# Performance work log

Measured on AMD Instinct MI355X. Metric: run time of the kernel, lower is better.

## Reference

```python
import jax, jax.numpy as jnp
import numpy as np

N = 50000
IN_C = 512
HID = 16
HEADS = 3
OUT_C = 128
NEG_SLOPE = 0.2


def _add_self_loops(edge_index, n):
    loop = jnp.arange(n, dtype=edge_index.dtype)
    src = jnp.concatenate([edge_index[0], loop])
    dst = jnp.concatenate([edge_index[1], loop])
    return src, dst


def gat_conv(x, W, a_src, a_dst, b, src, dst, n):
    # x: [N, Fin], W: [Fin, H*C], a_src/a_dst: [H, C], b: [H*C]
    H, C = a_src.shape
    h = (x @ W).reshape(n, H, C)                      # [N, H, C]
    e_src = jnp.einsum('nhc,hc->nh', h, a_src)        # [N, H]
    e_dst = jnp.einsum('nhc,hc->nh', h, a_dst)        # [N, H]
    e = jax.nn.leaky_relu(e_src[src] + e_dst[dst], NEG_SLOPE)  # [E, H]
    # segment softmax over incoming edges of each destination node
    m = jax.ops.segment_max(e, dst, num_segments=n)
    e = jnp.exp(e - m[dst])
    s = jax.ops.segment_sum(e, dst, num_segments=n)
    alpha = e / s[dst]                                 # [E, H]
    out = jax.ops.segment_sum(h[src] * alpha[:, :, None], dst, num_segments=n)
    return out.reshape(n, H * C) + b


def gcn_conv(x, W, b, src, dst, n):
    h = x @ W                                          # [N, Fout]
    ones = jnp.ones(src.shape[0], dtype=h.dtype)
    deg = jax.ops.segment_sum(ones, dst, num_segments=n)
    dinv = jax.lax.rsqrt(jnp.maximum(deg, 1.0))
    norm = dinv[src] * dinv[dst]                       # [E]
    out = jax.ops.segment_sum(h[src] * norm[:, None], dst, num_segments=n)
    return out + b


def setup_inputs() -> dict:
    key = jax.random.key(0)
    ks = jax.random.split(key, 16)
    E = 800000
    x = jax.random.normal(ks[0], (N, IN_C), dtype=jnp.float32)
    edge_index = jax.random.randint(ks[1], (2, E), 0, N, dtype=jnp.int64)

    def glorot(k, shape):
        fan = shape[0] + shape[-1]
        return jax.random.uniform(k, shape, jnp.float32, -1.0, 1.0) * np.sqrt(6.0 / fan)

    return {
        'x': x,
        'edge_index': edge_index,
        'W1': glorot(ks[2], (IN_C, HEADS * HID)),
        'a_src1': glorot(ks[3], (HEADS, HID)),
        'a_dst1': glorot(ks[4], (HEADS, HID)),
        'b1': jnp.zeros((HEADS * HID,), jnp.float32),
        'W2': glorot(ks[5], (HEADS * HID, OUT_C)),
        'a_src2': glorot(ks[6], (1, OUT_C)),
        'a_dst2': glorot(ks[7], (1, OUT_C)),
        'b2': jnp.zeros((OUT_C,), jnp.float32),
        'Wg': glorot(ks[8], (OUT_C, OUT_C)),
        'bg': jnp.zeros((OUT_C,), jnp.float32),
        'Wl': glorot(ks[9], (OUT_C, OUT_C)),
        'bl': jnp.zeros((OUT_C,), jnp.float32),
    }


def reference(x, edge_index, W1, a_src1, a_dst1, b1, W2, a_src2, a_dst2, b2, Wg, bg, Wl, bl):
    n = x.shape[0]
    src, dst = _add_self_loops(edge_index, n)
    # GATModel: gat1 (3 heads, concat) -> elu -> gat2 (1 head) -> log_softmax
    h = gat_conv(x, W1, a_src1, a_dst1, b1, src, dst, n)
    h = jax.nn.elu(h)
    h = gat_conv(h, W2, a_src2, a_dst2, b2, src, dst, n)
    h = jax.nn.log_softmax(h, axis=1)
    # GCN: only conv1 is used in its forward, followed by relu
    h = jax.nn.relu(gcn_conv(h, Wg, bg, src, dst, n))
    # Linear1
    return h @ Wl + bl
```

## Files before the change

kernel.cpp:

```cpp
#include <hip/hip_runtime.h>
#include <hip/hip_bf16.h>
#include <math.h>

#define NN 50000
#define EE 800000
#define ET 850000
#define NB 196
#define NEG 0.2f

static __device__ __forceinline__ float lrelu(float x){ return x > 0.f ? x : NEG * x; }
static __device__ __forceinline__ void edge_sd(const int* __restrict__ ei, int e, int& s, int& d){
  if (e < EE){ s = ei[e]; d = ei[e + EE]; } else { s = e - EE; d = s; }
}

__global__ __launch_bounds__(256) void k_hist(const int* __restrict__ ei, int* __restrict__ deg_i)
{
  int e = blockIdx.x * 256 + threadIdx.x;
  if (e >= ET) return;
  int s, d; edge_sd(ei, e, s, d);
  atomicAdd(deg_i + d, 1);
}

__global__ __launch_bounds__(256) void k_scan_part(const int* __restrict__ deg_i, int* __restrict__ bsum)
{
  __shared__ int wsum[4];
  int t = threadIdx.x;
  int i = blockIdx.x * 256 + t;
  int v = (i < NN) ? deg_i[i] : 0;
  int r = v;
#pragma unroll
  for (int off = 32; off; off >>= 1) r += __shfl_xor(r, off);
  if ((t & 63) == 0) wsum[t >> 6] = r;
  __syncthreads();
  if (t == 0) bsum[blockIdx.x] = wsum[0] + wsum[1] + wsum[2] + wsum[3];
}

__global__ __launch_bounds__(256) void k_scan_top(const int* __restrict__ bsum, int* __restrict__ boff)
{
  __shared__ int bs[256];
  int t = threadIdx.x;
  int v = (t < NB) ? bsum[t] : 0;
  bs[t] = v;
  __syncthreads();
  for (int off = 1; off < 256; off <<= 1){
    int add = (t >= off) ? bs[t - off] : 0;
    __syncthreads();
    bs[t] += add;
    __syncthreads();
  }
  if (t < NB) boff[t] = bs[t] - v;
}

__global__ __launch_bounds__(256) void k_scan_fin(const int* __restrict__ deg_i,
    const int* __restrict__ boff, int* __restrict__ row_start, float* __restrict__ dinv)
{
  __shared__ int bs[256];
  int t = threadIdx.x;
  int i = blockIdx.x * 256 + t;
  int v = (i < NN) ? deg_i[i] : 0;
  bs[t] = v;
  __syncthreads();
  for (int off = 1; off < 256; off <<= 1){
    int add = (t >= off) ? bs[t - off] : 0;
    __syncthreads();
    bs[t] += add;
    __syncthreads();
  }
  if (i < NN){
    row_start[i] = boff[blockIdx.x] + bs[t] - v;
    dinv[i] = rsqrtf(fmaxf((float)v, 1.0f));
  }
  if (i == 0) row_start[NN] = ET;
}

__global__ __launch_bounds__(256) void k_fill(const int* __restrict__ ei,
    const int* __restrict__ row_start, int* __restrict__ cur, int* __restrict__ csr)
{
  int e = blockIdx.x * 256 + threadIdx.x;
  if (e >= ET) return;
  int s, d; edge_sd(ei, e, s, d);
  int pos = atomicAdd(cur + d, 1);
  csr[row_start[d] + pos] = s;
}

__global__ __launch_bounds__(64) void k_w2(const float* __restrict__ W2,
    const float* __restrict__ as2, const float* __restrict__ ad2,
    float* __restrict__ w2as, float* __restrict__ w2ad)
{
  int k = threadIdx.x;
  if (k >= 48) return;
  float s = 0.f, d = 0.f;
  for (int j = 0; j < 128; ++j){
    float w = W2[(size_t)k * 128 + j];
    s = fmaf(w, as2[j], s);
    d = fmaf(w, ad2[j], d);
  }
  w2as[k] = s; w2ad[k] = d;
}

__global__ __launch_bounds__(256) void k_gat1_gemm(
    const float* __restrict__ x, const float* __restrict__ W1,
    const float* __restrict__ as1, const float* __restrict__ ad1,
    float* __restrict__ h1, float* __restrict__ es1, float* __restrict__ ed1)
{
  __shared__ float Xs[64][68];
  __shared__ float Bs[64][52];
  int t = threadIdx.x;
  int tx = t & 15, ty = t >> 4;
  int n0 = blockIdx.x * 64;
  float acc[4][3] = {};
  for (int kt = 0; kt < 512; kt += 64){
    __syncthreads();
#pragma unroll
    for (int p = 0; p < 4; ++p){
      int f = t + p * 256;
      int node = f >> 4, kq = f & 15;
      float4 v = make_float4(0.f, 0.f, 0.f, 0.f);
      int gn = n0 + node;
      if (gn < NN) v = *(const float4*)(x + (size_t)gn * 512 + kt + kq * 4);
      *(float4*)&Xs[node][kq * 4] = v;
    }
#pragma unroll
    for (int p = 0; p < 3; ++p){
      int f = t + p * 256;
      int k = f / 12, oq = f % 12;
      *(float4*)&Bs[k][oq * 4] = *(const float4*)(W1 + (size_t)(kt + k) * 48 + oq * 4);
    }
    __syncthreads();
#pragma unroll 4
    for (int k4 = 0; k4 < 64; k4 += 4){
      float4 q0 = *(const float4*)&Xs[ty * 4 + 0][k4];
      float4 q1 = *(const float4*)&Xs[ty * 4 + 1][k4];
      float4 q2 = *(const float4*)&Xs[ty * 4 + 2][k4];
      float4 q3 = *(const float4*)&Xs[ty * 4 + 3][k4];
      float a0[4] = {q0.x, q0.y, q0.z, q0.w};
      float a1[4] = {q1.x, q1.y, q1.z, q1.w};
      float a2[4] = {q2.x, q2.y, q2.z, q2.w};
      float a3[4] = {q3.x, q3.y, q3.z, q3.w};
#pragma unroll
      for (int kk = 0; kk < 4; ++kk){
        float b0 = Bs[k4 + kk][tx * 3 + 0];
        float b1 = Bs[k4 + kk][tx * 3 + 1];
        float b2 = Bs[k4 + kk][tx * 3 + 2];
        acc[0][0] = fmaf(a0[kk], b0, acc[0][0]); acc[0][1] = fmaf(a0[kk], b1, acc[0][1]); acc[0][2] = fmaf(a0[kk], b2, acc[0][2]);
        acc[1][0] = fmaf(a1[kk], b0, acc[1][0]); acc[1][1] = fmaf(a1[kk], b1, acc[1][1]); acc[1][2] = fmaf(a1[kk], b2, acc[1][2]);
        acc[2][0] = fmaf(a2[kk], b0, acc[2][0]); acc[2][1] = fmaf(a2[kk], b1, acc[2][1]); acc[2][2] = fmaf(a2[kk], b2, acc[2][2]);
        acc[3][0] = fmaf(a3[kk], b0, acc[3][0]); acc[3][1] = fmaf(a3[kk], b1, acc[3][1]); acc[3][2] = fmaf(a3[kk], b2, acc[3][2]);
      }
    }
  }
#pragma unroll
  for (int i = 0; i < 4; ++i){
    int gn = n0 + ty * 4 + i;
    float ps0 = 0.f, ps1 = 0.f, ps2 = 0.f, pd0 = 0.f, pd1 = 0.f, pd2 = 0.f;
#pragma unroll
    for (int j = 0; j < 3; ++j){
      int o = tx * 3 + j;
      int h = o >> 4;
      float a = acc[i][j];
      float vs = a * as1[o], vd = a * ad1[o];
      if (h == 0){ ps0 += vs; pd0 += vd; }
      else if (h == 1){ ps1 += vs; pd1 += vd; }
      else { ps2 += vs; pd2 += vd; }
    }
#pragma unroll
    for (int off = 1; off < 16; off <<= 1){
      ps0 += __shfl_xor(ps0, off, 16); ps1 += __shfl_xor(ps1, off, 16); ps2 += __shfl_xor(ps2, off, 16);
      pd0 += __shfl_xor(pd0, off, 16); pd1 += __shfl_xor(pd1, off, 16); pd2 += __shfl_xor(pd2, off, 16);
    }
    if (gn < NN){
      float* o = h1 + (size_t)gn * 48 + tx * 3;
      o[0] = acc[i][0]; o[1] = acc[i][1]; o[2] = acc[i][2];
      if (tx == 0){
        es1[(size_t)gn * 3 + 0] = ps0; es1[(size_t)gn * 3 + 1] = ps1; es1[(size_t)gn * 3 + 2] = ps2;
        ed1[(size_t)gn * 3 + 0] = pd0; ed1[(size_t)gn * 3 + 1] = pd1; ed1[(size_t)gn * 3 + 2] = pd2;
      }
    }
  }
}

__global__ __launch_bounds__(256) void k_gat1_agg(
    const int* __restrict__ csr, const int* __restrict__ row_start,
    const float* __restrict__ es1, const float* __restrict__ ed1,
    const float* __restrict__ h1, const float* __restrict__ b1,
    const float* __restrict__ w2as, const float* __restrict__ w2ad,
    float* __restrict__ o1, float* __restrict__ es2, float* __restrict__ ed2)
{
  int dn = (blockIdx.x * 256 + threadIdx.x) >> 6;
  int lane = threadIdx.x & 63;
  if (dn >= NN) return;
  bool act = lane < 48;
  int hd = act ? (lane >> 4) : 0;
  int beg = row_start[dn], end = row_start[dn + 1];
  float edv = ed1[(size_t)dn * 3 + hd];
  float m = -INFINITY, sum = 0.f, acc = 0.f;
  int i = beg;
  for (; i + 1 < end; i += 2){
    int s0 = csr[i], s1 = csr[i + 1];
    float e0 = lrelu(es1[(size_t)s0 * 3 + hd] + edv);
    float e1 = lrelu(es1[(size_t)s1 * 3 + hd] + edv);
    float h0 = act ? h1[(size_t)s0 * 48 + lane] : 0.f;
    float h1v = act ? h1[(size_t)s1 * 48 + lane] : 0.f;
    float mn = fmaxf(m, fmaxf(e0, e1));
    float sc = __expf(m - mn), w0 = __expf(e0 - mn), w1 = __expf(e1 - mn);
    sum = sum * sc + w0 + w1;
    acc = acc * sc + h0 * w0 + h1v * w1;
    m = mn;
  }
  if (i < end){
    int s0 = csr[i];
    float e0 = lrelu(es1[(size_t)s0 * 3 + hd] + edv);
    float h0 = act ? h1[(size_t)s0 * 48 + lane] : 0.f;
    float mn = fmaxf(m, e0);
    float sc = __expf(m - mn), w0 = __expf(e0 - mn);
    sum = sum * sc + w0;
    acc = acc * sc + h0 * w0;
  }
  float v = 0.f;
  if (act){
    v = acc / sum + b1[lane];
    v = v > 0.f ? v : expm1f(v);
    o1[(size_t)dn * 48 + lane] = v;
  }
  float ps = act ? v * w2as[lane] : 0.f;
  float pd = act ? v * w2ad[lane] : 0.f;
#pragma unroll
  for (int off = 32; off; off >>= 1){ ps += __shfl_xor(ps, off); pd += __shfl_xor(pd, off); }
  if (lane == 0){ es2[dn] = ps; ed2[dn] = pd; }
}

__global__ __launch_bounds__(256) void k_gat2_agg(
    const int* __restrict__ csr, const int* __restrict__ row_start,
    const float* __restrict__ es2, const float* __restrict__ ed2,
    const float* __restrict__ o1, float* __restrict__ agg2)
{
  int dn = (blockIdx.x * 256 + threadIdx.x) >> 6;
  int lane = threadIdx.x & 63;
  if (dn >= NN) return;
  bool act = lane < 48;
  int beg = row_start[dn], end = row_start[dn + 1];
  float edv = ed2[dn];
  float m = -INFINITY, sum = 0.f, acc = 0.f;
  int i = beg;
  for (; i + 1 < end; i += 2){
    int s0 = csr[i], s1 = csr[i + 1];
    float e0 = lrelu(es2[s0] + edv);
    float e1 = lrelu(es2[s1] + edv);
    float h0 = act ? o1[(size_t)s0 * 48 + lane] : 0.f;
    float h1v = act ? o1[(size_t)s1 * 48 + lane] : 0.f;
    float mn = fmaxf(m, fmaxf(e0, e1));
    float sc = __expf(m - mn), w0 = __expf(e0 - mn), w1 = __expf(e1 - mn);
    sum = sum * sc + w0 + w1;
    acc = acc * sc + h0 * w0 + h1v * w1;
    m = mn;
  }
  if (i < end){
    int s0 = csr[i];
    float e0 = lrelu(es2[s0] + edv);
    float h0 = act ? o1[(size_t)s0 * 48 + lane] : 0.f;
    float mn = fmaxf(m, e0);
    float sc = __expf(m - mn), w0 = __expf(e0 - mn);
    sum = sum * sc + w0;
    acc = acc * sc + h0 * w0;
  }
  if (act) agg2[(size_t)dn * 48 + lane] = acc / sum;
}

__global__ __launch_bounds__(256) void k_gat2_post(const float* __restrict__ agg2,
    const float* __restrict__ W2, const float* __restrict__ b2, float* __restrict__ o2)
{
  __shared__ float As[64][52];
  __shared__ float Ws[48][128];
  int t = threadIdx.x, tx = t & 15, ty = t >> 4;
  int n0 = blockIdx.x * 64;
#pragma unroll
  for (int p = 0; p < 3; ++p){
    int f = t + p * 256;
    int node = f / 12, kq = f % 12;
    float4 v = make_float4(0.f, 0.f, 0.f, 0.f);
    if (n0 + node < NN) v = *(const float4*)(agg2 + (size_t)(n0 + node) * 48 + kq * 4);
    *(float4*)&As[node][kq * 4] = v;
  }
#pragma unroll
  for (int p = 0; p < 6; ++p){
    int f = t + p * 256;
    int k = f >> 5, cq = f & 31;
    *(float4*)&Ws[k][cq * 4] = *(const float4*)(W2 + (size_t)k * 128 + cq * 4);
  }
  __syncthreads();
  float acc[4][8] = {};
#pragma unroll 4
  for (int k = 0; k < 48; ++k){
    float a0 = As[ty * 4 + 0][k];
    float a1 = As[ty * 4 + 1][k];
    float a2 = As[ty * 4 + 2][k];
    float a3 = As[ty * 4 + 3][k];
    float4 c0 = *(const float4*)&Ws[k][tx * 4];
    float4 c1 = *(const float4*)&Ws[k][tx * 4 + 64];
    float bv[8] = {c0.x, c0.y, c0.z, c0.w, c1.x, c1.y, c1.z, c1.w};
#pragma unroll
    for (int j = 0; j < 8; ++j){
      acc[0][j] = fmaf(a0, bv[j], acc[0][j]);
      acc[1][j] = fmaf(a1, bv[j], acc[1][j]);
      acc[2][j] = fmaf(a2, bv[j], acc[2][j]);
      acc[3][j] = fmaf(a3, bv[j], acc[3][j]);
    }
  }
  float bb[8];
#pragma unroll
  for (int j = 0; j < 4; ++j){ bb[j] = b2[tx * 4 + j]; bb[4 + j] = b2[64 + tx * 4 + j]; }
#pragma unroll
  for (int i = 0; i < 4; ++i){
    int gn = n0 + ty * 4 + i;
    float v[8];
#pragma unroll
    for (int j = 0; j < 8; ++j) v[j] = acc[i][j] + bb[j];
    float mx = v[0];
#pragma unroll
    for (int j = 1; j < 8; ++j) mx = fmaxf(mx, v[j]);
#pragma unroll
    for (int off = 1; off < 16; off <<= 1) mx = fmaxf(mx, __shfl_xor(mx, off, 16));
    float es = 0.f;
#pragma unroll
    for (int j = 0; j < 8; ++j) es += __expf(v[j] - mx);
#pragma unroll
    for (int off = 1; off < 16; off <<= 1) es += __shfl_xor(es, off, 16);
    float lse = mx + __logf(es);
    if (gn < NN){
      float4 o0 = make_float4(v[0] - lse, v[1] - lse, v[2] - lse, v[3] - lse);
      float4 o1v = make_float4(v[4] - lse, v[5] - lse, v[6] - lse, v[7] - lse);
      *(float4*)(o2 + (size_t)gn * 128 + tx * 4) = o0;
      *(float4*)(o2 + (size_t)gn * 128 + tx * 4 + 64) = o1v;
    }
  }
}

__global__ __launch_bounds__(256) void k_gcn_agg(
    const int* __restrict__ csr, const int* __restrict__ row_start,
    const float* __restrict__ dinv, const float* __restrict__ o2,
    float* __restrict__ aggD)
{
  int wid = (blockIdx.x * 256 + threadIdx.x) >> 6;
  int lane = threadIdx.x & 63;
  int half = lane >> 5, l32 = lane & 31;
  int d = wid * 2 + half;
  if (d >= NN) return;
  int beg = row_start[d], end = row_start[d + 1];
  float ax = 0.f, ay = 0.f, az = 0.f, aw = 0.f;
  float bx = 0.f, by = 0.f, bz = 0.f, bw = 0.f;
  int i = beg;
  for (; i + 1 < end; i += 2){
    int s0 = csr[i], s1 = csr[i + 1];
    float d0 = dinv[s0], d1 = dinv[s1];
    float4 v0 = *(const float4*)(o2 + (size_t)s0 * 128 + l32 * 4);
    float4 v1 = *(const float4*)(o2 + (size_t)s1 * 128 + l32 * 4);
    ax = fmaf(v0.x, d0, ax); ay = fmaf(v0.y, d0, ay); az = fmaf(v0.z, d0, az); aw = fmaf(v0.w, d0, aw);
    bx = fmaf(v1.x, d1, bx); by = fmaf(v1.y, d1, by); bz = fmaf(v1.z, d1, bz); bw = fmaf(v1.w, d1, bw);
  }
  if (i < end){
    int s0 = csr[i];
    float d0 = dinv[s0];
    float4 v0 = *(const float4*)(o2 + (size_t)s0 * 128 + l32 * 4);
    ax = fmaf(v0.x, d0, ax); ay = fmaf(v0.y, d0, ay); az = fmaf(v0.z, d0, az); aw = fmaf(v0.w, d0, aw);
  }
  float dd = dinv[d];
  float4 ov = make_float4((ax + bx) * dd, (ay + by) * dd, (az + bz) * dd, (aw + bw) * dd);
  *(float4*)(aggD + (size_t)d * 128 + l32 * 4) = ov;
}

__global__ __launch_bounds__(256) void k_final(const float* __restrict__ aggD,
    const float* __restrict__ Wg, const float* __restrict__ bg,
    const float* __restrict__ Wl, const float* __restrict__ bl,
    float* __restrict__ out)
{
  __shared__ float Ta[64][132];
  __shared__ float Ws[32][128];
  int t = threadIdx.x, tx = t & 15, ty = t >> 4;
  int n0 = blockIdx.x * 64;
#pragma unroll
  for (int p = 0; p < 8; ++p){
    int f = t + p * 256;
    int node = f >> 5, cq = f & 31;
    float4 v = make_float4(0.f, 0.f, 0.f, 0.f);
    if (n0 + node < NN) v = *(const float4*)(aggD + (size_t)(n0 + node) * 128 + cq * 4);
    *(float4*)&Ta[node][cq * 4] = v;
  }
  float accv[4][8];
  const float* Wcur = Wg;
  for (int ph = 0; ph < 2; ++ph){
#pragma unroll
    for (int i = 0; i < 4; ++i)
#pragma unroll
      for (int j = 0; j < 8; ++j) accv[i][j] = 0.f;
    for (int kt = 0; kt < 128; kt += 32){
      __syncthreads();
#pragma unroll
      for (int p = 0; p < 4; ++p){
        int f = t + p * 256;
        int k = f >> 5, cq = f & 31;
        *(float4*)&Ws[k][cq * 4] = *(const float4*)(Wcur + (size_t)(kt + k) * 128 + cq * 4);
      }
      __syncthreads();
#pragma unroll 4
      for (int k = 0; k < 32; ++k){
        float a0 = Ta[ty * 4 + 0][kt + k];
        float a1 = Ta[ty * 4 + 1][kt + k];
        float a2 = Ta[ty * 4 + 2][kt + k];
        float a3 = Ta[ty * 4 + 3][kt + k];
        float4 c0 = *(const float4*)&Ws[k][tx * 4];
        float4 c1 = *(const float4*)&Ws[k][tx * 4 + 64];
        float bv[8] = {c0.x, c0.y, c0.z, c0.w, c1.x, c1.y, c1.z, c1.w};
#pragma unroll
        for (int j = 0; j < 8; ++j){
          accv[0][j] = fmaf(a0, bv[j], accv[0][j]);
          accv[1][j] = fmaf(a1, bv[j], accv[1][j]);
          accv[2][j] = fmaf(a2, bv[j], accv[2][j]);
          accv[3][j] = fmaf(a3, bv[j], accv[3][j]);
        }
      }
    }
    if (ph == 0){
      __syncthreads();
#pragma unroll
      for (int i = 0; i < 4; ++i){
        int nloc = ty * 4 + i;
        float4 w0, w1;
        w0.x = fmaxf(accv[i][0] + bg[tx * 4 + 0], 0.f);
        w0.y = fmaxf(accv[i][1] + bg[tx * 4 + 1], 0.f);
        w0.z = fmaxf(accv[i][2] + bg[tx * 4 + 2], 0.f);
        w0.w = fmaxf(accv[i][3] + bg[tx * 4 + 3], 0.f);
        w1.x = fmaxf(accv[i][4] + bg[64 + tx * 4 + 0], 0.f);
        w1.y = fmaxf(accv[i][5] + bg[64 + tx * 4 + 1], 0.f);
        w1.z = fmaxf(accv[i][6] + bg[64 + tx * 4 + 2], 0.f);
        w1.w = fmaxf(accv[i][7] + bg[64 + tx * 4 + 3], 0.f);
        *(float4*)&Ta[nloc][tx * 4] = w0;
        *(float4*)&Ta[nloc][tx * 4 + 64] = w1;
      }
      Wcur = Wl;
    }
  }
#pragma unroll
  for (int i = 0; i < 4; ++i){
    int gn = n0 + ty * 4 + i;
    if (gn < NN){
      float4 o0, o1v;
      o0.x = accv[i][0] + bl[tx * 4 + 0];
      o0.y = accv[i][1] + bl[tx * 4 + 1];
      o0.z = accv[i][2] + bl[tx * 4 + 2];
      o0.w = accv[i][3] + bl[tx * 4 + 3];
      o1v.x = accv[i][4] + bl[64 + tx * 4 + 0];
      o1v.y = accv[i][5] + bl[64 + tx * 4 + 1];
      o1v.z = accv[i][6] + bl[64 + tx * 4 + 2];
      o1v.w = accv[i][7] + bl[64 + tx * 4 + 3];
      *(float4*)(out + (size_t)gn * 128 + tx * 4) = o0;
      *(float4*)(out + (size_t)gn * 128 + tx * 4 + 64) = o1v;
    }
  }
}

extern "C" void kernel_launch(void* const* d_in, const int* in_sizes, int n_in,
                              void* d_out, int out_size, void* d_ws, size_t ws_size,
                              hipStream_t stream)
{
  const float* x   = (const float*)d_in[0];
  const int*   ei  = (const int*)d_in[1];
  const float* W1  = (const float*)d_in[2];
  const float* as1 = (const float*)d_in[3];
  const float* ad1 = (const float*)d_in[4];
  const float* b1  = (const float*)d_in[5];
  const float* W2  = (const float*)d_in[6];
  const float* as2 = (const float*)d_in[7];
  const float* ad2 = (const float*)d_in[8];
  const float* b2  = (const float*)d_in[9];
  const float* Wg  = (const float*)d_in[10];
  const float* bg  = (const float*)d_in[11];
  const float* Wl  = (const float*)d_in[12];
  const float* bl  = (const float*)d_in[13];
  float* out = (float*)d_out;

  float* ws = (float*)d_ws;
  const size_t n = NN;
  float* h1   = ws;
  float* o1   = ws + 48 * n;
  float* agg2 = ws + 96 * n;
  float* o2   = ws + 144 * n;
  float* aggD = ws + 272 * n;
  float* es1  = ws + 400 * n;
  float* ed1  = ws + 403 * n;
  float* es2  = ws + 406 * n;
  float* ed2  = ws + 407 * n;
  float* dinv = ws + 408 * n;
  float* w2as = ws + 409 * n;
  float* w2ad = ws + 409 * n + 64;
  int* ints   = (int*)(ws + 410 * n);
  int* deg_i     = ints;
  int* cur       = ints + n;
  int* row_start = ints + 2 * n;
  int* csr       = ints + 3 * n + 1;
  int* bsum      = ints + 3 * n + 1 + ET;
  int* boff      = ints + 3 * n + 1 + ET + NB;

  hipMemsetAsync(deg_i, 0, 2 * n * sizeof(int), stream);

  const int egrid = (ET + 255) / 256;
  const int wgrid = (NN * 64) / 256;
  const int hgrid = (NN / 2 * 64) / 256;
  const int ggrid = (NN + 63) / 64;
  k_hist<<<egrid, 256, 0, stream>>>(ei, deg_i);
  k_scan_part<<<NB, 256, 0, stream>>>(deg_i, bsum);
  k_scan_top<<<1, 256, 0, stream>>>(bsum, boff);
  k_scan_fin<<<NB, 256, 0, stream>>>(deg_i, boff, row_start, dinv);
  k_fill<<<egrid, 256, 0, stream>>>(ei, row_start, cur, csr);
  k_w2<<<1, 64, 0, stream>>>(W2, as2, ad2, w2as, w2ad);
  k_gat1_gemm<<<ggrid, 256, 0, stream>>>(x, W1, as1, ad1, h1, es1, ed1);
  k_gat1_agg<<<wgrid, 256, 0, stream>>>(csr, row_start, es1, ed1, h1, b1, w2as, w2ad, o1, es2, ed2);
  k_gat2_agg<<<wgrid, 256, 0, stream>>>(csr, row_start, es2, ed2, o1, agg2);
  k_gat2_post<<<ggrid, 256, 0, stream>>>(agg2, W2, b2, o2);
  k_gcn_agg<<<hgrid, 256, 0, stream>>>(csr, row_start, dinv, o2, aggD);
  k_final<<<ggrid, 256, 0, stream>>>(aggD, Wg, bg, Wl, bl, out);
}
```

Baseline: 563.9 us.

## Prefetch GEMM tiles into registers, fold k_w2 into scan, init cursors from row_start

The GAT1 GEMM and the final two-GEMM kernel now load the next K tile from global memory into registers while the current shared-memory tile is being computed, to hide load latency. The final kernel's two phases are flattened into one 8-chunk loop so the prefetch carries across the switch from Wg to Wl. The W2·a projection moves into the single-block scan_top kernel, which removes one launch. The fill cursors now start at row_start, which drops one indexed load per edge and halves the memset. Register prefetching raises register pressure and may lower occupancy.

Result: slower. 599.1 us (+6.2%).

```diff
diff --git a/kernel.cpp b/kernel.cpp
--- a/kernel.cpp
+++ b/kernel.cpp
@@ -35,7 +35,9 @@
   if (t == 0) bsum[blockIdx.x] = wsum[0] + wsum[1] + wsum[2] + wsum[3];
 }
 
-__global__ __launch_bounds__(256) void k_scan_top(const int* __restrict__ bsum, int* __restrict__ boff)
+__global__ __launch_bounds__(256) void k_scan_top(const int* __restrict__ bsum, int* __restrict__ boff,
+    const float* __restrict__ W2, const float* __restrict__ as2, const float* __restrict__ ad2,
+    float* __restrict__ w2as, float* __restrict__ w2ad)
 {
   __shared__ int bs[256];
   int t = threadIdx.x;
@@ -49,10 +51,20 @@
     __syncthreads();
   }
   if (t < NB) boff[t] = bs[t] - v;
+  if (t < 48){
+    float s = 0.f, d = 0.f;
+    for (int j = 0; j < 128; ++j){
+      float w = W2[(size_t)t * 128 + j];
+      s = fmaf(w, as2[j], s);
+      d = fmaf(w, ad2[j], d);
+    }
+    w2as[t] = s; w2ad[t] = d;
+  }
 }
 
 __global__ __launch_bounds__(256) void k_scan_fin(const int* __restrict__ deg_i,
-    const int* __restrict__ boff, int* __restrict__ row_start, float* __restrict__ dinv)
+    const int* __restrict__ boff, int* __restrict__ row_start, int* __restrict__ cur,
+    float* __restrict__ dinv)
 {
   __shared__ int bs[256];
   int t = threadIdx.x;
@@ -67,35 +79,22 @@
     __syncthreads();
   }
   if (i < NN){
-    row_start[i] = boff[blockIdx.x] + bs[t] - v;
+    int rs = boff[blockIdx.x] + bs[t] - v;
+    row_start[i] = rs;
+    cur[i] = rs;
     dinv[i] = rsqrtf(fmaxf((float)v, 1.0f));
   }
   if (i == 0) row_start[NN] = ET;
 }
 
 __global__ __launch_bounds__(256) void k_fill(const int* __restrict__ ei,
-    const int* __restrict__ row_start, int* __restrict__ cur, int* __restrict__ csr)
+    int* __restrict__ cur, int* __restrict__ csr)
 {
   int e = blockIdx.x * 256 + threadIdx.x;
   if (e >= ET) return;
   int s, d; edge_sd(ei, e, s, d);
   int pos = atomicAdd(cur + d, 1);
-  csr[row_start[d] + pos] = s;
-}
-
-__global__ __launch_bounds__(64) void k_w2(const float* __restrict__ W2,
-    const float* __restrict__ as2, const float* __restrict__ ad2,
-    float* __restrict__ w2as, float* __restrict__ w2ad)
-{
-  int k = threadIdx.x;
-  if (k >= 48) return;
-  float s = 0.f, d = 0.f;
-  for (int j = 0; j < 128; ++j){
-    float w = W2[(size_t)k * 128 + j];
-    s = fmaf(w, as2[j], s);
-    d = fmaf(w, ad2[j], d);
-  }
-  w2as[k] = s; w2ad[k] = d;
+  csr[pos] = s;
 }
 
 __global__ __launch_bounds__(256) void k_gat1_gemm(
@@ -109,24 +108,43 @@
   int tx = t & 15, ty = t >> 4;
   int n0 = blockIdx.x * 64;
   float acc[4][3] = {};
+  int snode[4], skq[4];
+#pragma unroll
+  for (int p = 0; p < 4; ++p){ int f = t + p * 256; snode[p] = f >> 4; skq[p] = f & 15; }
+  int bk[3], boq[3];
+#pragma unroll
+  for (int p = 0; p < 3; ++p){ int f = t + p * 256; bk[p] = f / 12; boq[p] = f % 12; }
+
+  float4 px[4], pw[3];
+#pragma unroll
+  for (int p = 0; p < 4; ++p){
+    int gn = n0 + snode[p];
+    px[p] = (gn < NN) ? *(const float4*)(x + (size_t)gn * 512 + skq[p] * 4)
+                      : make_float4(0.f, 0.f, 0.f, 0.f);
+  }
+#pragma unroll
+  for (int p = 0; p < 3; ++p)
+    pw[p] = *(const float4*)(W1 + (size_t)bk[p] * 48 + boq[p] * 4);
+
   for (int kt = 0; kt < 512; kt += 64){
     __syncthreads();
 #pragma unroll
-    for (int p = 0; p < 4; ++p){
-      int f = t + p * 256;
-      int node = f >> 4, kq = f & 15;
-      float4 v = make_float4(0.f, 0.f, 0.f, 0.f);
-      int gn = n0 + node;
-      if (gn < NN) v = *(const float4*)(x + (size_t)gn * 512 + kt + kq * 4);
-      *(float4*)&Xs[node][kq * 4] = v;
-    }
-#pragma unroll
-    for (int p = 0; p < 3; ++p){
-      int f = t + p * 256;
-      int k = f / 12, oq = f % 12;
-      *(float4*)&Bs[k][oq * 4] = *(const float4*)(W1 + (size_t)(kt + k) * 48 + oq * 4);
-    }
-    __syncthreads();
+    for (int p = 0; p < 4; ++p) *(float4*)&Xs[snode[p]][skq[p] * 4] = px[p];
+#pragma unroll
+    for (int p = 0; p < 3; ++p) *(float4*)&Bs[bk[p]][boq[p] * 4] = pw[p];
+    __syncthreads();
+    if (kt + 64 < 512){
+      int ktn = kt + 64;
+#pragma unroll
+      for (int p = 0; p < 4; ++p){
+        int gn = n0 + snode[p];
+        px[p] = (gn < NN) ? *(const float4*)(x + (size_t)gn * 512 + ktn + skq[p] * 4)
+                          : make_float4(0.f, 0.f, 0.f, 0.f);
+      }
+#pragma unroll
+      for (int p = 0; p < 3; ++p)
+        pw[p] = *(const float4*)(W1 + (size_t)(ktn + bk[p]) * 48 + boq[p] * 4);
+    }
 #pragma unroll 4
     for (int k4 = 0; k4 < 64; k4 += 4){
       float4 q0 = *(const float4*)&Xs[ty * 4 + 0][k4];
@@ -385,41 +403,18 @@
     if (n0 + node < NN) v = *(const float4*)(aggD + (size_t)(n0 + node) * 128 + cq * 4);
     *(float4*)&Ta[node][cq * 4] = v;
   }
-  float accv[4][8];
-  const float* Wcur = Wg;
-  for (int ph = 0; ph < 2; ++ph){
-#pragma unroll
-    for (int i = 0; i < 4; ++i)
-#pragma unroll
-      for (int j = 0; j < 8; ++j) accv[i][j] = 0.f;
-    for (int kt = 0; kt < 128; kt += 32){
-      __syncthreads();
-#pragma unroll
-      for (int p = 0; p < 4; ++p){
-        int f = t + p * 256;
-        int k = f >> 5, cq = f & 31;
-        *(float4*)&Ws[k][cq * 4] = *(const float4*)(Wcur + (size_t)(kt + k) * 128 + cq * 4);
-      }
-      __syncthreads();
-#pragma unroll 4
-      for (int k = 0; k < 32; ++k){
-        float a0 = Ta[ty * 4 + 0][kt + k];
-        float a1 = Ta[ty * 4 + 1][kt + k];
-        float a2 = Ta[ty * 4 + 2][kt + k];
-        float a3 = Ta[ty * 4 + 3][kt + k];
-        float4 c0 = *(const float4*)&Ws[k][tx * 4];
-        float4 c1 = *(const float4*)&Ws[k][tx * 4 + 64];
-        float bv[8] = {c0.x, c0.y, c0.z, c0.w, c1.x, c1.y, c1.z, c1.w};
-#pragma unroll
-        for (int j = 0; j < 8; ++j){
-          accv[0][j] = fmaf(a0, bv[j], accv[0][j]);
-          accv[1][j] = fmaf(a1, bv[j], accv[1][j]);
-          accv[2][j] = fmaf(a2, bv[j], accv[2][j]);
-          accv[3][j] = fmaf(a3, bv[j], accv[3][j]);
-        }
-      }
-    }
-    if (ph == 0){
+  int wk[4], wcq[4];
+#pragma unroll
+  for (int p = 0; p < 4; ++p){ int f = t + p * 256; wk[p] = f >> 5; wcq[p] = f & 31; }
+
+  float accv[4][8] = {};
+  float4 pwv[4];
+#pragma unroll
+  for (int p = 0; p < 4; ++p) pwv[p] = *(const float4*)(Wg + (size_t)wk[p] * 128 + wcq[p] * 4);
+
+  for (int c = 0; c < 8; ++c){
+    int kt = (c & 3) * 32;
+    if (c == 4){
       __syncthreads();
 #pragma unroll
       for (int i = 0; i < 4; ++i){
@@ -436,7 +431,38 @@
         *(float4*)&Ta[nloc][tx * 4] = w0;
         *(float4*)&Ta[nloc][tx * 4 + 64] = w1;
       }
-      Wcur = Wl;
+#pragma unroll
+      for (int i = 0; i < 4; ++i)
+#pragma unroll
+        for (int j = 0; j < 8; ++j) accv[i][j] = 0.f;
+    }
+    __syncthreads();
+#pragma unroll
+    for (int p = 0; p < 4; ++p) *(float4*)&Ws[wk[p]][wcq[p] * 4] = pwv[p];
+    __syncthreads();
+    if (c < 7){
+      const float* Wn = (c + 1 < 4) ? Wg : Wl;
+      int ktn = ((c + 1) & 3) * 32;
+#pragma unroll
+      for (int p = 0; p < 4; ++p)
+        pwv[p] = *(const float4*)(Wn + (size_t)(ktn + wk[p]) * 128 + wcq[p] * 4);
+    }
+#pragma unroll 4
+    for (int k = 0; k < 32; ++k){
+      float a0 = Ta[ty * 4 + 0][kt + k];
+      float a1 = Ta[ty * 4 + 1][kt + k];
+      float a2 = Ta[ty * 4 + 2][kt + k];
+      float a3 = Ta[ty * 4 + 3][kt + k];
+      float4 c0 = *(const float4*)&Ws[k][tx * 4];
+      float4 c1 = *(const float4*)&Ws[k][tx * 4 + 64];
+      float bv[8] = {c0.x, c0.y, c0.z, c0.w, c1.x, c1.y, c1.z, c1.w};
+#pragma unroll
+      for (int j = 0; j < 8; ++j){
+        accv[0][j] = fmaf(a0, bv[j], accv[0][j]);
+        accv[1][j] = fmaf(a1, bv[j], accv[1][j]);
+        accv[2][j] = fmaf(a2, bv[j], accv[2][j]);
+        accv[3][j] = fmaf(a3, bv[j], accv[3][j]);
+      }
     }
   }
 #pragma unroll
@@ -500,7 +526,7 @@
   int* bsum      = ints + 3 * n + 1 + ET;
   int* boff      = ints + 3 * n + 1 + ET + NB;
 
-  hipMemsetAsync(deg_i, 0, 2 * n * sizeof(int), stream);
+  hipMemsetAsync(deg_i, 0, n * sizeof(int), stream);
 
   const int egrid = (ET + 255) / 256;
   const int wgrid = (NN * 64) / 256;
@@ -508,10 +534,9 @@
   const int ggrid = (NN + 63) / 64;
   k_hist<<<egrid, 256, 0, stream>>>(ei, deg_i);
   k_scan_part<<<NB, 256, 0, stream>>>(deg_i, bsum);
-  k_scan_top<<<1, 256, 0, stream>>>(bsum, boff);
-  k_scan_fin<<<NB, 256, 0, stream>>>(deg_i, boff, row_start, dinv);
-  k_fill<<<egrid, 256, 0, stream>>>(ei, row_start, cur, csr);
-  k_w2<<<1, 64, 0, stream>>>(W2, as2, ad2, w2as, w2ad);
+  k_scan_top<<<1, 256, 0, stream>>>(bsum, boff, W2, as2, ad2, w2as, w2ad);
+  k_scan_fin<<<NB, 256, 0, stream>>>(deg_i, boff, row_start, cur, dinv);
+  k_fill<<<egrid, 256, 0, stream>>>(ei, cur, csr);
   k_gat1_gemm<<<ggrid, 256, 0, stream>>>(x, W1, as1, ad1, h1, es1, ed1);
   k_gat1_agg<<<wgrid, 256, 0, stream>>>(csr, row_start, es1, ed1, h1, b1, w2as, w2ad, o1, es2, ed2);
   k_gat2_agg<<<wgrid, 256, 0, stream>>>(csr, row_start, es2, ed2, o1, agg2);
```
